# Kernel tuning notes

Measured on AMD Instinct MI355X. Metric: run time of the kernel, lower is better.

Reference implementation:

```python
import jax, jax.numpy as jnp
import numpy as np

DIM = 1024
HEADS = 16
WIN = 128          # local window size
BATCH = 4
SEQ = 4096
HEAD_DIM = DIM // HEADS
HIDDEN = 2 * DIM   # GEGLU hidden_dim = 2*dim
EPS = 1e-5
NEG_INF = -1e9


def layer_norm(x, g, b):
    m = jnp.mean(x, axis=-1, keepdims=True)
    v = jnp.mean((x - m) ** 2, axis=-1, keepdims=True)
    return (x - m) * jax.lax.rsqrt(v + EPS) * g + b


def sliding_causal_local_attn(x, wq, wk, wv, wo, bo, rel_bias):
    # x: [B, S, D]; sliding-window causal attention: each query attends to
    # its own window plus the previous window (look_backward=1), causally masked.
    B, S, D = x.shape
    h, w, dh = HEADS, WIN, HEAD_DIM
    nw = S // w
    scale = dh ** -0.5

    def split_heads(t):  # [B,S,D] -> [B,h,nw,w,dh]
        return t.reshape(B, S, h, dh).transpose(0, 2, 1, 3).reshape(B, h, nw, w, dh)

    q = split_heads(x @ wq)
    k = split_heads(x @ wk)
    v = split_heads(x @ wv)

    # context = [previous window ; current window] -> [B,h,nw,2w,dh]
    k_pad = jnp.pad(k, ((0, 0), (0, 0), (1, 0), (0, 0), (0, 0)))
    v_pad = jnp.pad(v, ((0, 0), (0, 0), (1, 0), (0, 0), (0, 0)))
    kc = jnp.concatenate([k_pad[:, :, :-1], k_pad[:, :, 1:]], axis=3)
    vc = jnp.concatenate([v_pad[:, :, :-1], v_pad[:, :, 1:]], axis=3)

    logits = jnp.einsum('bhnid,bhnjd->bhnij', q, kc) * scale  # [B,h,nw,w,2w]

    i = jnp.arange(w)[:, None]        # query pos within window
    j = jnp.arange(2 * w)[None, :]    # key pos within [prev;cur] context
    dist = i + w - j                  # relative distance, 0..2w-1 when causal
    causal = dist >= 0
    # learned relative position bias per head, indexed by distance
    bias = rel_bias[:, jnp.clip(dist, 0, 2 * w - 1)]  # [h, w, 2w]
    logits = logits + bias[None, :, None]

    n_idx = jnp.arange(nw)[:, None, None]
    valid = causal[None] & ((n_idx > 0) | (j[None] >= w))  # mask padded first window
    logits = jnp.where(valid[None, None], logits, NEG_INF)

    attn = jax.nn.softmax(logits, axis=-1)
    out = jnp.einsum('bhnij,bhnjd->bhnid', attn, vc)           # [B,h,nw,w,dh]
    out = out.reshape(B, h, S, dh).transpose(0, 2, 1, 3).reshape(B, S, D)
    return out @ wo + bo


def geglu(x, w1, b1, w2, b2):
    proj = x @ w1 + b1                         # [B,S,2*HIDDEN]
    val, gate = jnp.split(proj, 2, axis=-1)
    return (val * jax.nn.gelu(gate, approximate=False)) @ w2 + b2


def setup_inputs() -> dict:
    key = jax.random.key(0)
    ks = jax.random.split(key, 12)
    sd = 0.02
    return {
        'x': jax.random.normal(ks[0], (BATCH, SEQ, DIM), jnp.float32),
        'ln1_g': jnp.ones((DIM,), jnp.float32),
        'ln1_b': jnp.zeros((DIM,), jnp.float32),
        'ln2_g': jnp.ones((DIM,), jnp.float32),
        'ln2_b': jnp.zeros((DIM,), jnp.float32),
        'wq': jax.random.normal(ks[1], (DIM, DIM), jnp.float32) * sd,
        'wk': jax.random.normal(ks[2], (DIM, DIM), jnp.float32) * sd,
        'wv': jax.random.normal(ks[3], (DIM, DIM), jnp.float32) * sd,
        'wo': jax.random.normal(ks[4], (DIM, DIM), jnp.float32) * sd,
        'bo': jnp.zeros((DIM,), jnp.float32),
        'rel_bias': jax.random.normal(ks[5], (HEADS, 2 * WIN), jnp.float32) * sd,
        'w_ff1': jax.random.normal(ks[6], (DIM, 2 * HIDDEN), jnp.float32) * sd,
        'b_ff1': jnp.zeros((2 * HIDDEN,), jnp.float32),
        'w_ff2': jax.random.normal(ks[7], (HIDDEN, DIM), jnp.float32) * sd,
        'b_ff2': jnp.zeros((DIM,), jnp.float32),
    }


def reference(x, ln1_g, ln1_b, ln2_g, ln2_b, wq, wk, wv, wo, bo, rel_bias,
              w_ff1, b_ff1, w_ff2, b_ff2):
    x = x + sliding_causal_local_attn(layer_norm(x, ln1_g, ln1_b),
                                      wq, wk, wv, wo, bo, rel_bias)
    x = x + geglu(layer_norm(x, ln2_g, ln2_b), w_ff1, b_ff1, w_ff2, b_ff2)
    return x
```

## Files before the change

kernel.cpp:

```cpp
#include <hip/hip_runtime.h>
#include <math.h>

typedef __attribute__((ext_vector_type(8))) short s16x8;
typedef __attribute__((ext_vector_type(4))) float f32x4;

__device__ __forceinline__ float b2f(unsigned short u){
  unsigned int i = ((unsigned int)u) << 16;
  float f; __builtin_memcpy(&f, &i, 4); return f;
}
__device__ __forceinline__ unsigned short f2b(float f){
  unsigned int i; __builtin_memcpy(&i, &f, 4);
  unsigned int r = (i + 0x7fffu + ((i >> 16) & 1u)) >> 16;
  return (unsigned short)r;
}
__device__ __forceinline__ f32x4 mfma16(s16x8 a, s16x8 b, f32x4 c){
  return __builtin_amdgcn_mfma_f32_16x16x32_bf16(a, b, c, 0, 0, 0);
}
__device__ __forceinline__ float gelu_exact(float x){
  return 0.5f * x * (1.0f + erff(x * 0.70710678118654752f));
}
__device__ __forceinline__ void gl_lds16(const unsigned short* g, unsigned short* l){
  __builtin_amdgcn_global_load_lds(
      (const __attribute__((address_space(1))) unsigned int*)g,
      (__attribute__((address_space(3))) unsigned int*)l, 16, 0, 0);
}

__device__ __forceinline__ void ln_row(const float* __restrict__ xrow,
                                       const float* __restrict__ g,
                                       const float* __restrict__ b,
                                       unsigned short* __restrict__ orow, int lane){
  const float4* xr = (const float4*)xrow;
  float4 u[4];
  #pragma unroll
  for(int q = 0; q < 4; q++) u[q] = xr[lane + 64*q];
  float s = 0.0f, ss = 0.0f;
  #pragma unroll
  for(int q = 0; q < 4; q++){
    s  += u[q].x + u[q].y + u[q].z + u[q].w;
    ss += u[q].x*u[q].x + u[q].y*u[q].y + u[q].z*u[q].z + u[q].w*u[q].w;
  }
  #pragma unroll
  for(int o = 32; o; o >>= 1){ s += __shfl_xor(s, o, 64); ss += __shfl_xor(ss, o, 64); }
  float m = s * (1.0f/1024.0f);
  float inv = rsqrtf(ss * (1.0f/1024.0f) - m*m + 1e-5f);
  #pragma unroll
  for(int q = 0; q < 4; q++){
    float4 ug = ((const float4*)g)[lane + 64*q];
    float4 ub = ((const float4*)b)[lane + 64*q];
    ushort4 o4;
    o4.x = f2b((u[q].x - m) * inv * ug.x + ub.x);
    o4.y = f2b((u[q].y - m) * inv * ug.y + ub.y);
    o4.z = f2b((u[q].z - m) * inv * ug.z + ub.z);
    o4.w = f2b((u[q].w - m) * inv * ug.w + ub.w);
    ((ushort4*)orow)[lane + 64*q] = o4;
  }
}

__global__ __launch_bounds__(256) void prep_k(
    const float* __restrict__ x, const float* __restrict__ ln1_g, const float* __restrict__ ln1_b,
    unsigned short* __restrict__ h,
    const float* __restrict__ wq, const float* __restrict__ wk, const float* __restrict__ wv,
    const float* __restrict__ wo, const float* __restrict__ wff1, const float* __restrict__ wff2,
    unsigned short* __restrict__ wqkvT, unsigned short* __restrict__ woT,
    unsigned short* __restrict__ wff1T, unsigned short* __restrict__ wff2T)
{
  const int bz = blockIdx.x;
  if(bz >= 10240){
    int id = bz - 10240;
    int lane = threadIdx.x & 63, wave = threadIdx.x >> 6;
    int row = id * 4 + wave;
    ln_row(x + (size_t)row*1024, ln1_g, ln1_b, h + (size_t)row*1024, lane);
    return;
  }
  const float* in; unsigned short* out; int R, C, c0, r0;
  if(bz < 4096){
    int w = bz >> 10, id = bz & 1023;
    const float* srcs[4] = {wq, wk, wv, wo};
    unsigned short* dsts[4] = {wqkvT, wqkvT + 1048576, wqkvT + 2097152, woT};
    in = srcs[w]; out = dsts[w]; R = 1024; C = 1024;
    c0 = (id & 31) * 32; r0 = (id >> 5) * 32;
  } else if(bz < 8192){
    int id = bz - 4096;
    in = wff1; out = wff1T; R = 1024; C = 4096;
    c0 = (id & 127) * 32; r0 = (id >> 7) * 32;
  } else {
    int id = bz - 8192;
    in = wff2; out = wff2T; R = 2048; C = 1024;
    c0 = (id & 31) * 32; r0 = (id >> 5) * 32;
  }
  __shared__ unsigned short tile[32][33];
  int tx = threadIdx.x & 31, ty = threadIdx.x >> 5;
  #pragma unroll
  for(int i = 0; i < 4; i++)
    tile[ty + 8*i][tx] = f2b(in[(size_t)(r0 + ty + 8*i) * C + c0 + tx]);
  __syncthreads();
  #pragma unroll
  for(int i = 0; i < 4; i++)
    out[(size_t)(c0 + ty + 8*i) * R + r0 + tx] = tile[tx][ty + 8*i];
}

__global__ __launch_bounds__(256) void ln2_k(const float* __restrict__ x,
                                             const float* __restrict__ g,
                                             const float* __restrict__ b,
                                             unsigned short* __restrict__ out){
  int lane = threadIdx.x & 63, wave = threadIdx.x >> 6;
  int row = blockIdx.x * 4 + wave;
  ln_row(x + (size_t)row*1024, g, b, out + (size_t)row*1024, lane);
}

template<int MODE>
__global__ __launch_bounds__(512, 1) void gemm256(
    const unsigned short* __restrict__ A, const unsigned short* __restrict__ Bt,
    void* Cv, void* Cv2, int N, int n_split, int K,
    const float* __restrict__ bias, const float* __restrict__ res)
{
  __shared__ __align__(16) unsigned short As[2][256*64];
  __shared__ __align__(16) unsigned short Bs[2][256*64];

  int m_tile, n_tile;
  {
    unsigned int lin = blockIdx.y * gridDim.x + blockIdx.x;
    unsigned int mpx = gridDim.y >> 3;
    unsigned int xcd = lin & 7u, idx = lin >> 3;
    m_tile = xcd * mpx + (idx % mpx);
    n_tile = idx / mpx;
  }
  const int m0 = m_tile * 256;
  const int n0 = n_tile * (MODE == 1 ? 128 : 256);
  const int tid = threadIdx.x;
  const int wave = tid >> 6, lane = tid & 63;
  const int ln3 = lane >> 3;
  const int cg  = (lane & 7) ^ ln3;
  const int wm = (wave >> 2) * 128, wn = (wave & 3) * 64;
  const int lrow = lane & 15, quad = lane >> 4, xw = lrow & 7;

  const unsigned short* aSrc[4];
  const unsigned short* bSrc[4];
  #pragma unroll
  for(int hq = 0; hq < 4; hq++){
    int rt = hq*64 + wave*8 + ln3;
    aSrc[hq] = A + (size_t)(m0 + rt)*K + cg*8;
    int brow;
    if(MODE == 1){
      int grp = rt >> 4;
      brow = (grp & 1)*2048 + n0 + ((grp >> 1)*16) + (rt & 15);
    } else {
      brow = n0 + rt;
    }
    bSrc[hq] = Bt + (size_t)brow*K + cg*8;
  }

#define STAGE_A(bsel, hh, koff) do{ \
    gl_lds16(aSrc[(hh)*2+0] + (koff), &As[(bsel)][(hh)*8192 + wave*512]); \
    gl_lds16(aSrc[(hh)*2+1] + (koff), &As[(bsel)][(hh)*8192 + 4096 + wave*512]); }while(0)
#define STAGE_B(bsel, hh, koff) do{ \
    gl_lds16(bSrc[(hh)*2+0] + (koff), &Bs[(bsel)][(hh)*8192 + wave*512]); \
    gl_lds16(bSrc[(hh)*2+1] + (koff), &Bs[(bsel)][(hh)*8192 + 4096 + wave*512]); }while(0)
#define RD(buf, rowbase, kk) \
    (*(const s16x8*)&(buf)[((rowbase) + lrow)*64 + (((((kk)<<2)+quad)^xw)*8)])

  f32x4 acc[8][4];
  #pragma unroll
  for(int i = 0; i < 8; i++)
    #pragma unroll
    for(int j = 0; j < 4; j++)
      #pragma unroll
      for(int r = 0; r < 4; r++) acc[i][j][r] = 0.0f;

  STAGE_A(0,0,0); STAGE_A(0,1,0); STAGE_B(0,0,0); STAGE_B(0,1,0);

  s16x8 af[4][2], bf[4][2];
  const int nk = K >> 6;
  #pragma unroll 2
  for(int kt = 0; kt < nk; kt++){
    const int cur = kt & 1, nxt = cur ^ 1;
    const int koff = (kt + 1) << 6;
    const bool pf = (kt + 1 < nk);

    if(pf){ STAGE_A(nxt, 0, koff);
            asm volatile("s_waitcnt vmcnt(2)\n\ts_barrier" ::: "memory"); }
    else  { asm volatile("s_waitcnt vmcnt(0)\n\ts_barrier" ::: "memory"); }
    #pragma unroll
    for(int i = 0; i < 4; i++){ af[i][0] = RD(As[cur], wm + i*16, 0);
                                af[i][1] = RD(As[cur], wm + i*16, 1); }
    #pragma unroll
    for(int j = 0; j < 2; j++){ bf[j][0] = RD(Bs[cur], wn + j*16, 0);
                                bf[j][1] = RD(Bs[cur], wn + j*16, 1); }
    __builtin_amdgcn_s_setprio(1);
    #pragma unroll
    for(int i = 0; i < 4; i++)
      #pragma unroll
      for(int j = 0; j < 2; j++){
        acc[i][j] = mfma16(af[i][0], bf[j][0], acc[i][j]);
        acc[i][j] = mfma16(af[i][1], bf[j][1], acc[i][j]);
      }
    __builtin_amdgcn_s_setprio(0);

    if(pf) STAGE_A(nxt, 1, koff);
    #pragma unroll
    for(int j = 2; j < 4; j++){ bf[j][0] = RD(Bs[cur], wn + j*16, 0);
                                bf[j][1] = RD(Bs[cur], wn + j*16, 1); }
    __builtin_amdgcn_s_setprio(1);
    #pragma unroll
    for(int i = 0; i < 4; i++)
      #pragma unroll
      for(int j = 2; j < 4; j++){
        acc[i][j] = mfma16(af[i][0], bf[j][0], acc[i][j]);
        acc[i][j] = mfma16(af[i][1], bf[j][1], acc[i][j]);
      }
    __builtin_amdgcn_s_setprio(0);

    if(pf) STAGE_B(nxt, 0, koff);
    #pragma unroll
    for(int i = 0; i < 4; i++){ af[i][0] = RD(As[cur], wm + 64 + i*16, 0);
                                af[i][1] = RD(As[cur], wm + 64 + i*16, 1); }
    __builtin_amdgcn_s_setprio(1);
    #pragma unroll
    for(int i = 0; i < 4; i++)
      #pragma unroll
      for(int j = 0; j < 2; j++){
        acc[4+i][j] = mfma16(af[i][0], bf[j][0], acc[4+i][j]);
        acc[4+i][j] = mfma16(af[i][1], bf[j][1], acc[4+i][j]);
      }
    __builtin_amdgcn_s_setprio(0);

    if(pf) STAGE_B(nxt, 1, koff);
    __builtin_amdgcn_s_setprio(1);
    #pragma unroll
    for(int i = 0; i < 4; i++)
      #pragma unroll
      for(int j = 2; j < 4; j++){
        acc[4+i][j] = mfma16(af[i][0], bf[j][0], acc[4+i][j]);
        acc[4+i][j] = mfma16(af[i][1], bf[j][1], acc[4+i][j]);
      }
    __builtin_amdgcn_s_setprio(0);
    asm volatile("s_waitcnt lgkmcnt(0)\n\ts_barrier" ::: "memory");
  }
#undef STAGE_A
#undef STAGE_B
#undef RD

  const int qr = quad * 4;
  if(MODE == 1){
    unsigned short* C = (unsigned short*)Cv;
    const int a4 = wave & 3;
    #pragma unroll
    for(int i = 0; i < 8; i++){
      #pragma unroll
      for(int gp = 0; gp < 2; gp++){
        int colv = n0 + a4*32 + gp*16 + lrow;
        float bv = bias[colv];
        float bg = bias[2048 + colv];
        #pragma unroll
        for(int r = 0; r < 4; r++){
          size_t row = (size_t)(m0 + wm + i*16 + qr + r);
          float v  = acc[i][2*gp  ][r] + bv;
          float gt = acc[i][2*gp+1][r] + bg;
          C[row*2048 + colv] = f2b(v * gelu_exact(gt));
        }
      }
    }
  } else if(MODE == 0){
    unsigned short* C1 = (unsigned short*)Cv;
    unsigned short* C2 = (unsigned short*)Cv2;
    #pragma unroll
    for(int i = 0; i < 8; i++)
      #pragma unroll
      for(int j = 0; j < 4; j++){
        int col = n0 + wn + j*16 + lrow;
        #pragma unroll
        for(int r = 0; r < 4; r++){
          size_t row = (size_t)(m0 + wm + i*16 + qr + r);
          if(col < n_split) C1[row*n_split + col] = f2b(acc[i][j][r]);
          else              C2[row*(N - n_split) + (col - n_split)] = f2b(acc[i][j][r]);
        }
      }
  } else {
    float* C = (float*)Cv;
    #pragma unroll
    for(int i = 0; i < 8; i++)
      #pragma unroll
      for(int j = 0; j < 4; j++){
        int col = n0 + wn + j*16 + lrow;
        float bv = bias[col];
        #pragma unroll
        for(int r = 0; r < 4; r++){
          size_t row = (size_t)(m0 + wm + i*16 + qr + r);
          size_t idx = row * (size_t)N + col;
          C[idx] = acc[i][j][r] + bv + res[idx];
        }
      }
  }
}

__global__ __launch_bounds__(256, 1) void attn_k(const unsigned short* __restrict__ qk,
                                                 const unsigned short* __restrict__ vbuf,
                                                 const float* __restrict__ rel_bias,
                                                 unsigned short* __restrict__ attn_out)
{
  __shared__ unsigned short kvS[128 * 72];
  __shared__ unsigned short PS[128 * 136];
  __shared__ float biasS[256];

  const int n = blockIdx.x, h = blockIdx.y, b = blockIdx.z;
  const int tid = threadIdx.x;
  const int wave = tid >> 6, lane = tid & 63;
  const int lrow = lane & 15, quad = lane >> 4, lk = quad * 8;
  const int rbase = wave * 32;
  const size_t rowbase = (size_t)b * 4096;
  const int prev = (n > 0) ? (n - 1) : 0;

  biasS[tid] = rel_bias[h * 256 + tid];

  s16x8 aq[2][2];
  #pragma unroll
  for(int mi = 0; mi < 2; mi++)
    #pragma unroll
    for(int kk = 0; kk < 2; kk++)
      aq[mi][kk] = *(const s16x8*)&qk[(rowbase + n*128 + rbase + mi*16 + lrow)*2048
                                      + h*64 + kk*32 + lk];

  f32x4 lg[2][16];
  #pragma unroll
  for(int mi = 0; mi < 2; mi++)
    #pragma unroll
    for(int nj = 0; nj < 16; nj++)
      #pragma unroll
      for(int r = 0; r < 4; r++) lg[mi][nj][r] = 0.0f;

  for(int jh = 0; jh < 2; jh++){
    if(jh) __syncthreads();
    #pragma unroll
    for(int it = 0; it < 4; it++){
      int cid = tid + it * 256;
      int jloc = cid >> 3, c8 = (cid & 7) * 8;
      int j = jh * 128 + jloc;
      int srow = (j < 128) ? (prev*128 + j) : (n*128 + j - 128);
      *(s16x8*)&kvS[jloc*72 + c8] =
        *(const s16x8*)&qk[(rowbase + srow)*2048 + 1024 + h*64 + c8];
    }
    __syncthreads();
    #pragma unroll
    for(int njl = 0; njl < 8; njl++){
      #pragma unroll
      for(int kk = 0; kk < 2; kk++){
        s16x8 bk = *(const s16x8*)&kvS[(njl*16 + lrow)*72 + kk*32 + lk];
        #pragma unroll
        for(int mi = 0; mi < 2; mi++)
          lg[mi][jh*8 + njl] = mfma16(aq[mi][kk], bk, lg[mi][jh*8 + njl]);
      }
    }
  }
  __syncthreads();

  #pragma unroll
  for(int mi = 0; mi < 2; mi++){
    #pragma unroll
    for(int r = 0; r < 4; r++){
      int i = rbase + mi*16 + quad*4 + r;
      float mx = -3e38f;
      #pragma unroll
      for(int nj = 0; nj < 16; nj++){
        int j = nj*16 + lrow;
        int dist = i + 128 - j;
        bool valid = (dist >= 0) && ((n > 0) || (j >= 128));
        float l = valid ? (lg[mi][nj][r] * 0.125f + biasS[dist & 255]) : -1e9f;
        lg[mi][nj][r] = l;
        mx = fmaxf(mx, l);
      }
      #pragma unroll
      for(int o = 1; o < 16; o <<= 1) mx = fmaxf(mx, __shfl_xor(mx, o, 64));
      float s = 0.0f;
      #pragma unroll
      for(int nj = 0; nj < 16; nj++){
        float p = __expf(lg[mi][nj][r] - mx);
        lg[mi][nj][r] = p;
        s += p;
      }
      #pragma unroll
      for(int o = 1; o < 16; o <<= 1) s += __shfl_xor(s, o, 64);
      float inv = 1.0f / s;
      #pragma unroll
      for(int nj = 0; nj < 16; nj++) lg[mi][nj][r] *= inv;
    }
  }

  f32x4 o_acc[2][4];
  #pragma unroll
  for(int mi = 0; mi < 2; mi++)
    #pragma unroll
    for(int nj = 0; nj < 4; nj++)
      #pragma unroll
      for(int r = 0; r < 4; r++) o_acc[mi][nj][r] = 0.0f;

  for(int jh = 0; jh < 2; jh++){
    {
      int jloc = tid >> 1;
      int dbase = (tid & 1) * 32;
      int j = jh * 128 + jloc;
      int srow = (j < 128) ? (prev*128 + j) : (n*128 + j - 128);
      const unsigned short* vr = &vbuf[(rowbase + srow)*1024 + h*64 + dbase];
      #pragma unroll
      for(int i8 = 0; i8 < 4; i8++){
        s16x8 vv = *(const s16x8*)&vr[i8 * 8];
        #pragma unroll
        for(int e = 0; e < 8; e++)
          kvS[(dbase + i8*8 + e)*136 + jloc] = (unsigned short)vv[e];
      }
    }
    #pragma unroll
    for(int mi = 0; mi < 2; mi++)
      #pragma unroll
      for(int r = 0; r < 4; r++)
        #pragma unroll
        for(int njl = 0; njl < 8; njl++)
          PS[(rbase + mi*16 + quad*4 + r)*136 + njl*16 + lrow] = f2b(lg[mi][jh*8 + njl][r]);
    __syncthreads();
    #pragma unroll
    for(int kk = 0; kk < 4; kk++){
      s16x8 ap[2];
      #pragma unroll
      for(int mi = 0; mi < 2; mi++)
        ap[mi] = *(const s16x8*)&PS[(rbase + mi*16 + lrow)*136 + kk*32 + lk];
      #pragma unroll
      for(int nj = 0; nj < 4; nj++){
        s16x8 bv = *(const s16x8*)&kvS[(nj*16 + lrow)*136 + kk*32 + lk];
        #pragma unroll
        for(int mi = 0; mi < 2; mi++)
          o_acc[mi][nj] = mfma16(ap[mi], bv, o_acc[mi][nj]);
      }
    }
    __syncthreads();
  }

  #pragma unroll
  for(int mi = 0; mi < 2; mi++)
    #pragma unroll
    for(int nj = 0; nj < 4; nj++)
      #pragma unroll
      for(int r = 0; r < 4; r++){
        size_t row = rowbase + n*128 + rbase + mi*16 + quad*4 + r;
        int col = h*64 + nj*16 + lrow;
        attn_out[row * 1024 + col] = f2b(o_acc[mi][nj][r]);
      }
}

extern "C" void kernel_launch(void* const* d_in, const int* in_sizes, int n_in,
                              void* d_out, int out_size, void* d_ws, size_t ws_size,
                              hipStream_t stream) {
  const float* x     = (const float*)d_in[0];
  const float* ln1_g = (const float*)d_in[1];
  const float* ln1_b = (const float*)d_in[2];
  const float* ln2_g = (const float*)d_in[3];
  const float* ln2_b = (const float*)d_in[4];
  const float* wq    = (const float*)d_in[5];
  const float* wk    = (const float*)d_in[6];
  const float* wv    = (const float*)d_in[7];
  const float* wo    = (const float*)d_in[8];
  const float* bo    = (const float*)d_in[9];
  const float* rel   = (const float*)d_in[10];
  const float* wff1  = (const float*)d_in[11];
  const float* bff1  = (const float*)d_in[12];
  const float* wff2  = (const float*)d_in[13];
  const float* bff2  = (const float*)d_in[14];
  float* out = (float*)d_out;
  char*  ws  = (char*)d_ws;

  unsigned short* wqkvT = (unsigned short*)(ws);
  unsigned short* woT   = (unsigned short*)(ws +  6291456);
  unsigned short* wff1T = (unsigned short*)(ws +  8388608);
  unsigned short* wff2T = (unsigned short*)(ws + 16777216);
  unsigned short* h     = (unsigned short*)(ws + 20971520);
  unsigned short* qk    = (unsigned short*)(ws + 54525952);
  unsigned short* ff    = qk;
  unsigned short* vbuf  = (unsigned short*)d_out;
  float*          x1    = out;

  prep_k<<<14336, 256, 0, stream>>>(x, ln1_g, ln1_b, h,
                                    wq, wk, wv, wo, wff1, wff2,
                                    wqkvT, woT, wff1T, wff2T);
  gemm256<0><<<dim3(12, 64), 512, 0, stream>>>(h, wqkvT, qk, vbuf, 3072, 2048, 1024,
                                               nullptr, nullptr);
  attn_k<<<dim3(32, 16, 4), 256, 0, stream>>>(qk, vbuf, rel, h);
  gemm256<2><<<dim3(4, 64), 512, 0, stream>>>(h, woT, x1, nullptr, 1024, 0, 1024,
                                              bo, x);
  ln2_k<<<4096, 256, 0, stream>>>(x1, ln2_g, ln2_b, h);
  gemm256<1><<<dim3(16, 64), 512, 0, stream>>>(h, wff1T, ff, nullptr, 2048, 0, 1024,
                                               bff1, nullptr);
  gemm256<2><<<dim3(4, 64), 512, 0, stream>>>(ff, wff2T, out, nullptr, 1024, 0, 2048,
                                              bff2, x1);
}
```

Measured before the change: 730.9 us.

## Reschedule GEMM main loop by k-half with finer barriers and hoist MODE0 store split

```diff
diff --git a/kernel.cpp b/kernel.cpp
--- a/kernel.cpp
+++ b/kernel.cpp
@@ -169,7 +169,7 @@
 
   STAGE_A(0,0,0); STAGE_A(0,1,0); STAGE_B(0,0,0); STAGE_B(0,1,0);
 
-  s16x8 af[4][2], bf[4][2];
+  s16x8 af[4], bfv[4][2];
   const int nk = K >> 6;
   #pragma unroll 2
   for(int kt = 0; kt < nk; kt++){
@@ -180,61 +180,61 @@
     if(pf){ STAGE_A(nxt, 0, koff);
             asm volatile("s_waitcnt vmcnt(2)\n\ts_barrier" ::: "memory"); }
     else  { asm volatile("s_waitcnt vmcnt(0)\n\ts_barrier" ::: "memory"); }
-    #pragma unroll
-    for(int i = 0; i < 4; i++){ af[i][0] = RD(As[cur], wm + i*16, 0);
-                                af[i][1] = RD(As[cur], wm + i*16, 1); }
-    #pragma unroll
-    for(int j = 0; j < 2; j++){ bf[j][0] = RD(Bs[cur], wn + j*16, 0);
-                                bf[j][1] = RD(Bs[cur], wn + j*16, 1); }
+
+    #pragma unroll
+    for(int i = 0; i < 4; i++) af[i]     = RD(As[cur], wm + i*16, 0);
+    #pragma unroll
+    for(int j = 0; j < 4; j++) bfv[j][0] = RD(Bs[cur], wn + j*16, 0);
+    asm volatile("s_waitcnt lgkmcnt(0)" ::: "memory");
     __builtin_amdgcn_s_setprio(1);
     #pragma unroll
     for(int i = 0; i < 4; i++)
       #pragma unroll
-      for(int j = 0; j < 2; j++){
-        acc[i][j] = mfma16(af[i][0], bf[j][0], acc[i][j]);
-        acc[i][j] = mfma16(af[i][1], bf[j][1], acc[i][j]);
-      }
+      for(int j = 0; j < 4; j++)
+        acc[i][j] = mfma16(af[i], bfv[j][0], acc[i][j]);
     __builtin_amdgcn_s_setprio(0);
-
+    asm volatile("s_barrier" ::: "memory");
+
+    #pragma unroll
+    for(int i = 0; i < 4; i++) af[i]     = RD(As[cur], wm + i*16, 1);
+    #pragma unroll
+    for(int j = 0; j < 4; j++) bfv[j][1] = RD(Bs[cur], wn + j*16, 1);
     if(pf) STAGE_A(nxt, 1, koff);
-    #pragma unroll
-    for(int j = 2; j < 4; j++){ bf[j][0] = RD(Bs[cur], wn + j*16, 0);
-                                bf[j][1] = RD(Bs[cur], wn + j*16, 1); }
+    asm volatile("s_barrier\n\ts_waitcnt lgkmcnt(0)" ::: "memory");
     __builtin_amdgcn_s_setprio(1);
     #pragma unroll
     for(int i = 0; i < 4; i++)
       #pragma unroll
-      for(int j = 2; j < 4; j++){
-        acc[i][j] = mfma16(af[i][0], bf[j][0], acc[i][j]);
-        acc[i][j] = mfma16(af[i][1], bf[j][1], acc[i][j]);
-      }
+      for(int j = 0; j < 4; j++)
+        acc[i][j] = mfma16(af[i], bfv[j][1], acc[i][j]);
     __builtin_amdgcn_s_setprio(0);
-
+    asm volatile("s_barrier" ::: "memory");
+
+    #pragma unroll
+    for(int i = 0; i < 4; i++) af[i] = RD(As[cur], wm + 64 + i*16, 0);
     if(pf) STAGE_B(nxt, 0, koff);
-    #pragma unroll
-    for(int i = 0; i < 4; i++){ af[i][0] = RD(As[cur], wm + 64 + i*16, 0);
-                                af[i][1] = RD(As[cur], wm + 64 + i*16, 1); }
+    asm volatile("s_barrier\n\ts_waitcnt lgkmcnt(0)" ::: "memory");
     __builtin_amdgcn_s_setprio(1);
     #pragma unroll
     for(int i = 0; i < 4; i++)
       #pragma unroll
-      for(int j = 0; j < 2; j++){
-        acc[4+i][j] = mfma16(af[i][0], bf[j][0], acc[4+i][j]);
-        acc[4+i][j] = mfma16(af[i][1], bf[j][1], acc[4+i][j]);
-      }
+      for(int j = 0; j < 4; j++)
+        acc[4+i][j] = mfma16(af[i], bfv[j][0], acc[4+i][j]);
     __builtin_amdgcn_s_setprio(0);
-
+    asm volatile("s_barrier" ::: "memory");
+
+    #pragma unroll
+    for(int i = 0; i < 4; i++) af[i] = RD(As[cur], wm + 64 + i*16, 1);
     if(pf) STAGE_B(nxt, 1, koff);
+    asm volatile("s_barrier\n\ts_waitcnt lgkmcnt(0)" ::: "memory");
     __builtin_amdgcn_s_setprio(1);
     #pragma unroll
     for(int i = 0; i < 4; i++)
       #pragma unroll
-      for(int j = 2; j < 4; j++){
-        acc[4+i][j] = mfma16(af[i][0], bf[j][0], acc[4+i][j]);
-        acc[4+i][j] = mfma16(af[i][1], bf[j][1], acc[4+i][j]);
-      }
+      for(int j = 0; j < 4; j++)
+        acc[4+i][j] = mfma16(af[i], bfv[j][1], acc[4+i][j]);
     __builtin_amdgcn_s_setprio(0);
-    asm volatile("s_waitcnt lgkmcnt(0)\n\ts_barrier" ::: "memory");
+    asm volatile("s_barrier" ::: "memory");
   }
 #undef STAGE_A
 #undef STAGE_B
@@ -261,18 +261,19 @@
       }
     }
   } else if(MODE == 0){
-    unsigned short* C1 = (unsigned short*)Cv;
-    unsigned short* C2 = (unsigned short*)Cv2;
+    const bool left = (n0 + 256) <= n_split;
+    unsigned short* Cb = left ? (unsigned short*)Cv : (unsigned short*)Cv2;
+    const int stride = left ? n_split : (N - n_split);
+    const int cb0 = left ? n0 : (n0 - n_split);
     #pragma unroll
     for(int i = 0; i < 8; i++)
       #pragma unroll
       for(int j = 0; j < 4; j++){
-        int col = n0 + wn + j*16 + lrow;
+        int col = cb0 + wn + j*16 + lrow;
         #pragma unroll
         for(int r = 0; r < 4; r++){
           size_t row = (size_t)(m0 + wm + i*16 + qr + r);
-          if(col < n_split) C1[row*n_split + col] = f2b(acc[i][j][r]);
-          else              C2[row*(N - n_split) + (col - n_split)] = f2b(acc[i][j][r]);
+          Cb[row*stride + col] = f2b(acc[i][j][r]);
         }
       }
   } else {
```

Result: no change. 738.9 us (+1.1%).

## Make GEMM persistent with cross-tile prefetch of the next tile's first K-slice

Applied to the files above, without the earlier changes.

```diff
diff --git a/kernel.cpp b/kernel.cpp
--- a/kernel.cpp
+++ b/kernel.cpp
@@ -112,50 +112,67 @@
 __global__ __launch_bounds__(512, 1) void gemm256(
     const unsigned short* __restrict__ A, const unsigned short* __restrict__ Bt,
     void* Cv, void* Cv2, int N, int n_split, int K,
-    const float* __restrict__ bias, const float* __restrict__ res)
+    const float* __restrict__ bias, const float* __restrict__ res, int ntpb)
 {
   __shared__ __align__(16) unsigned short As[2][256*64];
   __shared__ __align__(16) unsigned short Bs[2][256*64];
 
-  int m_tile, n_tile;
-  {
-    unsigned int lin = blockIdx.y * gridDim.x + blockIdx.x;
-    unsigned int mpx = gridDim.y >> 3;
-    unsigned int xcd = lin & 7u, idx = lin >> 3;
-    m_tile = xcd * mpx + (idx % mpx);
-    n_tile = idx / mpx;
-  }
-  const int m0 = m_tile * 256;
-  const int n0 = n_tile * (MODE == 1 ? 128 : 256);
+  const int p = blockIdx.x;
   const int tid = threadIdx.x;
   const int wave = tid >> 6, lane = tid & 63;
   const int ln3 = lane >> 3;
   const int cg  = (lane & 7) ^ ln3;
   const int wm = (wave >> 2) * 128, wn = (wave & 3) * 64;
   const int lrow = lane & 15, quad = lane >> 4, xw = lrow & 7;
-
-  const unsigned short* aSrc[4];
-  const unsigned short* bSrc[4];
-  #pragma unroll
-  for(int hq = 0; hq < 4; hq++){
-    int rt = hq*64 + wave*8 + ln3;
-    aSrc[hq] = A + (size_t)(m0 + rt)*K + cg*8;
-    int brow;
-    if(MODE == 1){
-      int grp = rt >> 4;
-      brow = (grp & 1)*2048 + n0 + ((grp >> 1)*16) + (rt & 15);
+  const int nk = K >> 6;
+
+  auto tmn = [&](int o, int& m0, int& n0){
+    unsigned int lin = (unsigned int)p + ((unsigned int)o << 8);
+    unsigned int xcd = lin & 7u, idx = lin >> 3;
+    m0 = (int)(xcd * 8u + (idx & 7u)) * 256;
+    n0 = (int)(idx >> 3) * (MODE == 1 ? 128 : 256);
+  };
+
+  const unsigned short* aP[4];
+  const unsigned short* bP[4];
+  auto setp = [&](int m0, int n0){
+    #pragma unroll
+    for(int hq = 0; hq < 4; hq++){
+      int rt = hq*64 + wave*8 + ln3;
+      aP[hq] = A + (size_t)(m0 + rt)*K + cg*8;
+      int brow;
+      if(MODE == 1){
+        int grp = rt >> 4;
+        brow = (grp & 1)*2048 + n0 + ((grp >> 1) << 4) + (rt & 15);
+      } else {
+        brow = n0 + rt;
+      }
+      bP[hq] = Bt + (size_t)brow*K + cg*8;
+    }
+  };
+
+  int os = 0, ks = 0;
+  auto adv = [&](){
+    ++ks;
+    if(ks == nk){
+      ks = 0; ++os;
+      if(os < ntpb){ int m0n, n0n; tmn(os, m0n, n0n); setp(m0n, n0n); }
     } else {
-      brow = n0 + rt;
-    }
-    bSrc[hq] = Bt + (size_t)brow*K + cg*8;
-  }
-
-#define STAGE_A(bsel, hh, koff) do{ \
-    gl_lds16(aSrc[(hh)*2+0] + (koff), &As[(bsel)][(hh)*8192 + wave*512]); \
-    gl_lds16(aSrc[(hh)*2+1] + (koff), &As[(bsel)][(hh)*8192 + 4096 + wave*512]); }while(0)
-#define STAGE_B(bsel, hh, koff) do{ \
-    gl_lds16(bSrc[(hh)*2+0] + (koff), &Bs[(bsel)][(hh)*8192 + wave*512]); \
-    gl_lds16(bSrc[(hh)*2+1] + (koff), &Bs[(bsel)][(hh)*8192 + 4096 + wave*512]); }while(0)
+      aP[0] += 64; aP[1] += 64; aP[2] += 64; aP[3] += 64;
+      bP[0] += 64; bP[1] += 64; bP[2] += 64; bP[3] += 64;
+    }
+  };
+
+#define STAGE8(bsel) do{ \
+    gl_lds16(aP[0], &As[bsel][             wave*512]); \
+    gl_lds16(aP[1], &As[bsel][      4096 + wave*512]); \
+    gl_lds16(aP[2], &As[bsel][ 8192      + wave*512]); \
+    gl_lds16(aP[3], &As[bsel][ 8192+4096 + wave*512]); \
+    gl_lds16(bP[0], &Bs[bsel][             wave*512]); \
+    gl_lds16(bP[1], &Bs[bsel][      4096 + wave*512]); \
+    gl_lds16(bP[2], &Bs[bsel][ 8192      + wave*512]); \
+    gl_lds16(bP[3], &Bs[bsel][ 8192+4096 + wave*512]); \
+  }while(0)
 #define RD(buf, rowbase, kk) \
     (*(const s16x8*)&(buf)[((rowbase) + lrow)*64 + (((((kk)<<2)+quad)^xw)*8)])
 
@@ -167,130 +184,116 @@
       #pragma unroll
       for(int r = 0; r < 4; r++) acc[i][j][r] = 0.0f;
 
-  STAGE_A(0,0,0); STAGE_A(0,1,0); STAGE_B(0,0,0); STAGE_B(0,1,0);
-
-  s16x8 af[4][2], bf[4][2];
-  const int nk = K >> 6;
-  #pragma unroll 2
-  for(int kt = 0; kt < nk; kt++){
-    const int cur = kt & 1, nxt = cur ^ 1;
-    const int koff = (kt + 1) << 6;
-    const bool pf = (kt + 1 < nk);
-
-    if(pf){ STAGE_A(nxt, 0, koff);
-            asm volatile("s_waitcnt vmcnt(2)\n\ts_barrier" ::: "memory"); }
-    else  { asm volatile("s_waitcnt vmcnt(0)\n\ts_barrier" ::: "memory"); }
-    #pragma unroll
-    for(int i = 0; i < 4; i++){ af[i][0] = RD(As[cur], wm + i*16, 0);
-                                af[i][1] = RD(As[cur], wm + i*16, 1); }
-    #pragma unroll
-    for(int j = 0; j < 2; j++){ bf[j][0] = RD(Bs[cur], wn + j*16, 0);
-                                bf[j][1] = RD(Bs[cur], wn + j*16, 1); }
-    __builtin_amdgcn_s_setprio(1);
-    #pragma unroll
-    for(int i = 0; i < 4; i++)
-      #pragma unroll
-      for(int j = 0; j < 2; j++){
-        acc[i][j] = mfma16(af[i][0], bf[j][0], acc[i][j]);
-        acc[i][j] = mfma16(af[i][1], bf[j][1], acc[i][j]);
-      }
-    __builtin_amdgcn_s_setprio(0);
-
-    if(pf) STAGE_A(nxt, 1, koff);
-    #pragma unroll
-    for(int j = 2; j < 4; j++){ bf[j][0] = RD(Bs[cur], wn + j*16, 0);
-                                bf[j][1] = RD(Bs[cur], wn + j*16, 1); }
-    __builtin_amdgcn_s_setprio(1);
-    #pragma unroll
-    for(int i = 0; i < 4; i++)
-      #pragma unroll
-      for(int j = 2; j < 4; j++){
-        acc[i][j] = mfma16(af[i][0], bf[j][0], acc[i][j]);
-        acc[i][j] = mfma16(af[i][1], bf[j][1], acc[i][j]);
-      }
-    __builtin_amdgcn_s_setprio(0);
-
-    if(pf) STAGE_B(nxt, 0, koff);
-    #pragma unroll
-    for(int i = 0; i < 4; i++){ af[i][0] = RD(As[cur], wm + 64 + i*16, 0);
-                                af[i][1] = RD(As[cur], wm + 64 + i*16, 1); }
-    __builtin_amdgcn_s_setprio(1);
-    #pragma unroll
-    for(int i = 0; i < 4; i++)
-      #pragma unroll
-      for(int j = 0; j < 2; j++){
-        acc[4+i][j] = mfma16(af[i][0], bf[j][0], acc[4+i][j]);
-        acc[4+i][j] = mfma16(af[i][1], bf[j][1], acc[4+i][j]);
-      }
-    __builtin_amdgcn_s_setprio(0);
-
-    if(pf) STAGE_B(nxt, 1, koff);
-    __builtin_amdgcn_s_setprio(1);
-    #pragma unroll
-    for(int i = 0; i < 4; i++)
-      #pragma unroll
-      for(int j = 2; j < 4; j++){
-        acc[4+i][j] = mfma16(af[i][0], bf[j][0], acc[4+i][j]);
-        acc[4+i][j] = mfma16(af[i][1], bf[j][1], acc[4+i][j]);
-      }
-    __builtin_amdgcn_s_setprio(0);
+  int m0c, n0c; tmn(0, m0c, n0c);
+  int oc = 0, ktc = 0;
+
+  setp(m0c, n0c);
+  STAGE8(0);
+  adv();
+
+  s16x8 af[4], bfv[4][2];
+  const int tot = ntpb * nk;
+  for(int j = 0; j < tot; ++j){
+    const int cur = j & 1, nxt = cur ^ 1;
+    if(j + 1 < tot){
+      STAGE8(nxt);
+      asm volatile("s_waitcnt vmcnt(8)\n\ts_barrier" ::: "memory");
+      adv();
+    } else {
+      asm volatile("s_waitcnt vmcnt(0)\n\ts_barrier" ::: "memory");
+    }
+
+    const unsigned short* bA = &As[cur][0];
+    const unsigned short* bB = &Bs[cur][0];
+    #pragma unroll
+    for(int half = 0; half < 2; half++){
+      const int rb = wm + half*64;
+      #pragma unroll
+      for(int kk = 0; kk < 2; kk++){
+        #pragma unroll
+        for(int i = 0; i < 4; i++) af[i] = RD(bA, rb + i*16, kk);
+        if(half == 0){
+          #pragma unroll
+          for(int j4 = 0; j4 < 4; j4++) bfv[j4][kk] = RD(bB, wn + j4*16, kk);
+        }
+        __builtin_amdgcn_s_setprio(1);
+        #pragma unroll
+        for(int i = 0; i < 4; i++)
+          #pragma unroll
+          for(int j4 = 0; j4 < 4; j4++)
+            acc[half*4 + i][j4] = mfma16(af[i], bfv[j4][kk], acc[half*4 + i][j4]);
+        __builtin_amdgcn_s_setprio(0);
+      }
+    }
     asm volatile("s_waitcnt lgkmcnt(0)\n\ts_barrier" ::: "memory");
-  }
-#undef STAGE_A
-#undef STAGE_B
+
+    ++ktc;
+    if(ktc == nk){
+      ktc = 0;
+      const int qr = quad * 4;
+      if(MODE == 1){
+        unsigned short* C = (unsigned short*)Cv;
+        const int a4 = wave & 3;
+        #pragma unroll
+        for(int i = 0; i < 8; i++){
+          #pragma unroll
+          for(int gp = 0; gp < 2; gp++){
+            int colv = n0c + a4*32 + gp*16 + lrow;
+            float bv = bias[colv];
+            float bg = bias[2048 + colv];
+            #pragma unroll
+            for(int r = 0; r < 4; r++){
+              size_t row = (size_t)(m0c + wm + i*16 + qr + r);
+              float v  = acc[i][2*gp  ][r] + bv;
+              float gt = acc[i][2*gp+1][r] + bg;
+              C[row*2048 + colv] = f2b(v * gelu_exact(gt));
+            }
+          }
+        }
+      } else if(MODE == 0){
+        const bool left = (n0c + 256) <= n_split;
+        unsigned short* Cb = left ? (unsigned short*)Cv : (unsigned short*)Cv2;
+        const int stride = left ? n_split : (N - n_split);
+        const int cb0 = left ? n0c : (n0c - n_split);
+        #pragma unroll
+        for(int i = 0; i < 8; i++)
+          #pragma unroll
+          for(int j4 = 0; j4 < 4; j4++){
+            int col = cb0 + wn + j4*16 + lrow;
+            #pragma unroll
+            for(int r = 0; r < 4; r++){
+              size_t row = (size_t)(m0c + wm + i*16 + qr + r);
+              Cb[row*stride + col] = f2b(acc[i][j4][r]);
+            }
+          }
+      } else {
+        float* C = (float*)Cv;
+        #pragma unroll
+        for(int i = 0; i < 8; i++)
+          #pragma unroll
+          for(int j4 = 0; j4 < 4; j4++){
+            int col = n0c + wn + j4*16 + lrow;
+            float bv = bias[col];
+            #pragma unroll
+            for(int r = 0; r < 4; r++){
+              size_t row = (size_t)(m0c + wm + i*16 + qr + r);
+              size_t idx = row * (size_t)N + col;
+              C[idx] = acc[i][j4][r] + bv + res[idx];
+            }
+          }
+      }
+      #pragma unroll
+      for(int i = 0; i < 8; i++)
+        #pragma unroll
+        for(int j4 = 0; j4 < 4; j4++)
+          #pragma unroll
+          for(int r = 0; r < 4; r++) acc[i][j4][r] = 0.0f;
+      ++oc;
+      if(oc < ntpb) tmn(oc, m0c, n0c);
+    }
+  }
+#undef STAGE8
 #undef RD
-
-  const int qr = quad * 4;
-  if(MODE == 1){
-    unsigned short* C = (unsigned short*)Cv;
-    const int a4 = wave & 3;
-    #pragma unroll
-    for(int i = 0; i < 8; i++){
-      #pragma unroll
-      for(int gp = 0; gp < 2; gp++){
-        int colv = n0 + a4*32 + gp*16 + lrow;
-        float bv = bias[colv];
-        float bg = bias[2048 + colv];
-        #pragma unroll
-        for(int r = 0; r < 4; r++){
-          size_t row = (size_t)(m0 + wm + i*16 + qr + r);
-          float v  = acc[i][2*gp  ][r] + bv;
-          float gt = acc[i][2*gp+1][r] + bg;
-          C[row*2048 + colv] = f2b(v * gelu_exact(gt));
-        }
-      }
-    }
-  } else if(MODE == 0){
-    unsigned short* C1 = (unsigned short*)Cv;
-    unsigned short* C2 = (unsigned short*)Cv2;
-    #pragma unroll
-    for(int i = 0; i < 8; i++)
-      #pragma unroll
-      for(int j = 0; j < 4; j++){
-        int col = n0 + wn + j*16 + lrow;
-        #pragma unroll
-        for(int r = 0; r < 4; r++){
-          size_t row = (size_t)(m0 + wm + i*16 + qr + r);
-          if(col < n_split) C1[row*n_split + col] = f2b(acc[i][j][r]);
-          else              C2[row*(N - n_split) + (col - n_split)] = f2b(acc[i][j][r]);
-        }
-      }
-  } else {
-    float* C = (float*)Cv;
-    #pragma unroll
-    for(int i = 0; i < 8; i++)
-      #pragma unroll
-      for(int j = 0; j < 4; j++){
-        int col = n0 + wn + j*16 + lrow;
-        float bv = bias[col];
-        #pragma unroll
-        for(int r = 0; r < 4; r++){
-          size_t row = (size_t)(m0 + wm + i*16 + qr + r);
-          size_t idx = row * (size_t)N + col;
-          C[idx] = acc[i][j][r] + bv + res[idx];
-        }
-      }
-  }
 }
 
 __global__ __launch_bounds__(256, 1) void attn_k(const unsigned short* __restrict__ qk,
@@ -479,14 +482,14 @@
   prep_k<<<14336, 256, 0, stream>>>(x, ln1_g, ln1_b, h,
                                     wq, wk, wv, wo, wff1, wff2,
                                     wqkvT, woT, wff1T, wff2T);
-  gemm256<0><<<dim3(12, 64), 512, 0, stream>>>(h, wqkvT, qk, vbuf, 3072, 2048, 1024,
-                                               nullptr, nullptr);
+  gemm256<0><<<256, 512, 0, stream>>>(h, wqkvT, qk, vbuf, 3072, 2048, 1024,
+                                      nullptr, nullptr, 3);
   attn_k<<<dim3(32, 16, 4), 256, 0, stream>>>(qk, vbuf, rel, h);
-  gemm256<2><<<dim3(4, 64), 512, 0, stream>>>(h, woT, x1, nullptr, 1024, 0, 1024,
-                                              bo, x);
+  gemm256<2><<<256, 512, 0, stream>>>(h, woT, x1, nullptr, 1024, 0, 1024,
+                                      bo, x, 1);
   ln2_k<<<4096, 256, 0, stream>>>(x1, ln2_g, ln2_b, h);
-  gemm256<1><<<dim3(16, 64), 512, 0, stream>>>(h, wff1T, ff, nullptr, 2048, 0, 1024,
-                                               bff1, nullptr);
-  gemm256<2><<<dim3(4, 64), 512, 0, stream>>>(ff, wff2T, out, nullptr, 1024, 0, 2048,
-                                              bff2, x1);
-}
+  gemm256<1><<<256, 512, 0, stream>>>(h, wff1T, ff, nullptr, 2048, 0, 1024,
+                                      bff1, nullptr, 4);
+  gemm256<2><<<256, 512, 0, stream>>>(ff, wff2T, out, nullptr, 1024, 0, 2048,
+                                      bff2, x1, 1);
+}
```

New measurement: 740.6 us. About the same (+1.3%).
